# Performance work log

Measured on AMD Instinct MI355X. Metric: run time of the kernel, lower is better.

Reference implementation:

```python
import jax, jax.numpy as jnp
import numpy as np

N = 100000       # nodes
E = 1600000      # edges (avg degree 16)
F_IN = 20        # NUM_FEATURES
H = 128          # hidden_channels
EPS = 1e-5       # GraphNorm eps


def setup_inputs() -> dict:
    key = jax.random.key(0)
    ks = jax.random.split(key, 24)
    s = 0.05
    inp = {
        "x": jax.random.normal(ks[0], (N, F_IN), jnp.float32),
        "edge_index": jax.random.randint(ks[1], (2, E), 0, N, dtype=jnp.int32),
    }
    # SAGEConv params: lin_l (neighbors, with bias), lin_r (root, no bias)
    dims = [(F_IN, H), (H, H), (H, H)]
    k = 2
    for i, (din, dout) in enumerate(dims):
        inp[f"Wl{i}"] = jax.random.normal(ks[k], (dout, din), jnp.float32) * s; k += 1
        inp[f"bl{i}"] = jnp.zeros((dout,), jnp.float32)
        inp[f"Wr{i}"] = jax.random.normal(ks[k], (dout, din), jnp.float32) * s; k += 1
        # GraphNorm: weight, bias, mean_scale (alpha)
        inp[f"gw{i}"] = jnp.ones((dout,), jnp.float32)
        inp[f"gb{i}"] = jnp.zeros((dout,), jnp.float32)
        inp[f"ga{i}"] = jnp.ones((dout,), jnp.float32)
    # MLP head: 128 -> 64 -> 32 -> 1
    inp["hW1"] = jax.random.normal(ks[k], (64, H), jnp.float32) * s; k += 1
    inp["hb1"] = jnp.zeros((64,), jnp.float32)
    inp["hW2"] = jax.random.normal(ks[k], (32, 64), jnp.float32) * s; k += 1
    inp["hb2"] = jnp.zeros((32,), jnp.float32)
    inp["hW3"] = jax.random.normal(ks[k], (1, 32), jnp.float32) * s; k += 1
    inp["hb3"] = jnp.zeros((1,), jnp.float32)
    return inp


def _sage(x, src, dst, Wl, bl, Wr):
    # mean aggregation of source features at destination nodes
    deg = jax.ops.segment_sum(jnp.ones((src.shape[0],), x.dtype), dst, num_segments=N)
    agg = jax.ops.segment_sum(x[src], dst, num_segments=N)
    agg = agg / jnp.maximum(deg, 1.0)[:, None]
    return agg @ Wl.T + bl + x @ Wr.T


def _graphnorm(x, w, b, a):
    # single graph (batch=None): stats over all nodes, per channel
    mean = jnp.mean(x, axis=0)
    c = x - a * mean
    var = jnp.mean(c * c, axis=0)
    return w * c * jax.lax.rsqrt(var + EPS) + b


def reference(x, edge_index,
              Wl0, bl0, Wr0, gw0, gb0, ga0,
              Wl1, bl1, Wr1, gw1, gb1, ga1,
              Wl2, bl2, Wr2, gw2, gb2, ga2,
              hW1, hb1, hW2, hb2, hW3, hb3):
    src, dst = edge_index[0], edge_index[1]
    layers = [(Wl0, bl0, Wr0, gw0, gb0, ga0),
              (Wl1, bl1, Wr1, gw1, gb1, ga1),
              (Wl2, bl2, Wr2, gw2, gb2, ga2)]
    h = x
    for (Wl, bl, Wr, gw, gb, ga) in layers:
        h = _sage(h, src, dst, Wl, bl, Wr)
        h = _graphnorm(h, gw, gb, ga)
        h = jax.nn.gelu(h, approximate=False)  # dropout: eval mode (identity)
    h = jax.nn.gelu(h @ hW1.T + hb1, approximate=False)
    h = jax.nn.gelu(h @ hW2.T + hb2, approximate=False)
    out = jax.nn.sigmoid(h @ hW3.T + hb3)
    return out.squeeze(-1)  # [N]
```

## Files before the change

kernel.cpp:

```cpp
#include <hip/hip_runtime.h>
#include <hip/hip_bf16.h>
#include <math.h>

#define NN 100000
#define EE 1600000
#define FIN 20
#define HH 128
#define NBUK 391
#define FILLB 196
#define MMB 782

typedef __attribute__((ext_vector_type(8))) short bf16x8;
typedef __attribute__((ext_vector_type(4))) float f32x4;

__device__ __forceinline__ unsigned short f2b(float x) {
    unsigned int b = __float_as_uint(x);
    unsigned int r = b + 0x7fffu + ((b >> 16) & 1u);
    return (unsigned short)(r >> 16);
}
__device__ __forceinline__ float lof(unsigned int u) { return __uint_as_float(u << 16); }
__device__ __forceinline__ float hif(unsigned int u) { return __uint_as_float(u & 0xffff0000u); }
__device__ __forceinline__ unsigned int pk2(float a, float b) {
    return (unsigned int)f2b(a) | ((unsigned int)f2b(b) << 16);
}

__device__ __forceinline__ float gelu_exact(float z) {
    return 0.5f * z * (1.0f + erff(z * 0.70710678118654752f));
}

__global__ __launch_bounds__(256) void kb_cnt(const int* __restrict__ dst,
                                              int* __restrict__ bcnt) {
    __shared__ int c[NBUK];
    int t = threadIdx.x;
    for (int i = t; i < NBUK; i += 256) c[i] = 0;
    __syncthreads();
    int e0 = blockIdx.x * 8192;
    #pragma unroll 4
    for (int i = 0; i < 32; ++i) {
        int e = e0 + i * 256 + t;
        if (e < EE) atomicAdd(&c[dst[e] >> 8], 1);
    }
    __syncthreads();
    for (int i = t; i < NBUK; i += 256) if (c[i]) atomicAdd(&bcnt[i], c[i]);
}

__global__ void kb_scan(const int* __restrict__ bcnt, int* __restrict__ bbase,
                        int* __restrict__ cursor) {
    __shared__ int sh[512];
    int t = threadIdx.x;
    int v = (t < NBUK) ? bcnt[t] : 0;
    sh[t] = v;
    __syncthreads();
    for (int off = 1; off < 512; off <<= 1) {
        int add = (t >= off) ? sh[t - off] : 0;
        __syncthreads();
        sh[t] += add;
        __syncthreads();
    }
    if (t < NBUK) {
        int ex = sh[t] - v;
        bbase[t] = ex;
        cursor[t] = ex;
    }
    if (t == NBUK - 1) bbase[NBUK] = sh[t];
}

__global__ __launch_bounds__(256) void kb_fill(const int* __restrict__ src,
        const int* __restrict__ dst, int* __restrict__ cursor,
        unsigned int* __restrict__ pairs) {
    __shared__ int cnt[NBUK], base[NBUK], boff[NBUK];
    int t = threadIdx.x;
    for (int i = t; i < NBUK; i += 256) { cnt[i] = 0; boff[i] = 0; }
    __syncthreads();
    int e0 = blockIdx.x * 8192;
    #pragma unroll 4
    for (int i = 0; i < 32; ++i) {
        int e = e0 + i * 256 + t;
        if (e < EE) atomicAdd(&cnt[dst[e] >> 8], 1);
    }
    __syncthreads();
    for (int i = t; i < NBUK; i += 256)
        if (cnt[i]) base[i] = atomicAdd(&cursor[i], cnt[i]);
    __syncthreads();
    #pragma unroll 4
    for (int i = 0; i < 32; ++i) {
        int e = e0 + i * 256 + t;
        if (e < EE) {
            int d = dst[e];
            int b = d >> 8;
            int pos = base[b] + atomicAdd(&boff[b], 1);
            pairs[pos] = (unsigned int)src[e] | ((unsigned int)(d & 255) << 17);
        }
    }
}

__global__ __launch_bounds__(256) void kb_csr(const unsigned int* __restrict__ pairs,
        const int* __restrict__ bbase, int* __restrict__ row_start,
        int* __restrict__ deg, float* __restrict__ invdeg, int* __restrict__ col) {
    __shared__ int ldeg[256];
    __shared__ int lcnt[256];
    int b = blockIdx.x, t = threadIdx.x;
    int e0 = bbase[b], e1 = bbase[b + 1];
    ldeg[t] = 0;
    lcnt[t] = 0;
    __syncthreads();
    for (int e = e0 + t; e < e1; e += 256) atomicAdd(&ldeg[pairs[e] >> 17], 1);
    __syncthreads();
    int d = ldeg[t];
    for (int off = 1; off < 256; off <<= 1) {
        int add = (t >= off) ? ldeg[t - off] : 0;
        __syncthreads();
        ldeg[t] += add;
        __syncthreads();
    }
    int n = b * 256 + t;
    if (n < NN) {
        row_start[n] = e0 + ldeg[t] - d;
        deg[n] = d;
        invdeg[n] = 1.0f / fmaxf((float)d, 1.0f);
    }
    __syncthreads();
    for (int e = e0 + t; e < e1; e += 256) {
        unsigned int p = pairs[e];
        int dL = p >> 17;
        int pos = e0 + (dL ? ldeg[dL - 1] : 0) + atomicAdd(&lcnt[dL], 1);
        col[pos] = (int)(p & 0x1FFFFu);
    }
}

#define XB_N  (NN * 32)
#define A0_N  (NN * 64)
#define PACK_TOTAL (XB_N + A0_N + 8192 + 32768 + 32768 + 8192 + 2048 + 64 + 32)
__global__ __launch_bounds__(256) void k_pack_all(const float* __restrict__ x,
        const float* __restrict__ Wl0, const float* __restrict__ Wr0,
        const float* __restrict__ Wl1, const float* __restrict__ Wr1,
        const float* __restrict__ Wl2, const float* __restrict__ Wr2,
        const float* __restrict__ hW1, const float* __restrict__ hW2,
        const float* __restrict__ hb1, const float* __restrict__ hb2,
        unsigned short* __restrict__ xb, unsigned short* __restrict__ A0,
        unsigned short* __restrict__ Wt0, unsigned short* __restrict__ Wt2a,
        unsigned short* __restrict__ Wt2b, unsigned short* __restrict__ W1b,
        unsigned short* __restrict__ W2b, float* __restrict__ bH1,
        float* __restrict__ bH2) {
    int id = blockIdx.x * 256 + threadIdx.x;
    if (id < XB_N) {
        int n = id >> 5, k = id & 31;
        xb[id] = f2b((k < FIN) ? x[n * FIN + k] : 0.0f);
        return;
    }
    id -= XB_N;
    if (id < A0_N) {
        int k = id & 63;
        if (k >= FIN) {
            int n = id >> 6;
            float v = (k >= 32 && k < 32 + FIN) ? x[n * FIN + (k - 32)] : 0.0f;
            A0[id] = f2b(v);
        }
        return;
    }
    id -= A0_N;
    if (id < 8192) {
        int c = id >> 6, k = id & 63;
        float v = 0.0f;
        if (k < FIN) v = Wl0[c * FIN + k];
        else if (k >= 32 && k < 32 + FIN) v = Wr0[c * FIN + (k - 32)];
        Wt0[id] = f2b(v);
        return;
    }
    id -= 8192;
    if (id < 32768) {
        int c = id >> 8, k = id & 255;
        Wt2a[id] = f2b((k < HH) ? Wl1[c * HH + k] : Wr1[c * HH + (k - HH)]);
        return;
    }
    id -= 32768;
    if (id < 32768) {
        int c = id >> 8, k = id & 255;
        Wt2b[id] = f2b((k < HH) ? Wl2[c * HH + k] : Wr2[c * HH + (k - HH)]);
        return;
    }
    id -= 32768;
    if (id < 8192) { W1b[id] = f2b(hW1[id]); return; }
    id -= 8192;
    if (id < 2048) { W2b[id] = f2b(hW2[id]); return; }
    id -= 2048;
    if (id < 64) { bH1[id] = hb1[id]; return; }
    id -= 64;
    if (id < 32) { bH2[id] = hb2[id]; return; }
}

__global__ __launch_bounds__(256) void k_agg0(const uint2* __restrict__ xb2,
        const int* __restrict__ rs, const int* __restrict__ deg,
        const float* __restrict__ inv, const int* __restrict__ col,
        unsigned short* __restrict__ A0) {
    int wid = threadIdx.x >> 6;
    int lane = threadIdx.x & 63;
    int er = lane >> 3;
    int c8 = lane & 7;
    int n = blockIdx.x * 4 + wid;
    if (n >= NN) return;
    int s = rs[n], d = deg[n];
    float a0 = 0.f, a1 = 0.f, a2 = 0.f, a3 = 0.f;
    for (int j0 = 0; j0 < d; j0 += 8) {
        int j = j0 + er;
        if (j < d) {
            int c = col[s + j];
            uint2 v = xb2[(size_t)c * 8 + c8];
            a0 += lof(v.x); a1 += hif(v.x);
            a2 += lof(v.y); a3 += hif(v.y);
        }
    }
    #pragma unroll
    for (int m = 8; m < 64; m <<= 1) {
        a0 += __shfl_xor(a0, m, 64);
        a1 += __shfl_xor(a1, m, 64);
        a2 += __shfl_xor(a2, m, 64);
        a3 += __shfl_xor(a3, m, 64);
    }
    if (er == 0 && c8 < 5) {
        float iv = inv[n];
        uint2 o;
        o.x = pk2(a0 * iv, a1 * iv);
        o.y = pk2(a2 * iv, a3 * iv);
        ((uint2*)A0)[(size_t)n * 16 + c8] = o;
    }
}

__global__ __launch_bounds__(256) void k_aggb(const unsigned short* __restrict__ hB,
        const int* __restrict__ rs, const int* __restrict__ deg,
        const float* __restrict__ inv, const int* __restrict__ col,
        unsigned short* __restrict__ aggB) {
    int wid = threadIdx.x >> 6;
    int lane = threadIdx.x & 63;
    int er = lane >> 4;
    int c16 = lane & 15;
    int n = blockIdx.x * 4 + wid;
    if (n >= NN) return;
    int s = rs[n], d = deg[n];
    const uint4* h4 = (const uint4*)hB;
    float a0 = 0.f, a1 = 0.f, a2 = 0.f, a3 = 0.f;
    float a4 = 0.f, a5 = 0.f, a6 = 0.f, a7 = 0.f;
    for (int j0 = 0; j0 < d; j0 += 8) {
        #pragma unroll
        for (int u = 0; u < 2; ++u) {
            int j = j0 + u * 4 + er;
            if (j < d) {
                int c = col[s + j];
                uint4 v = h4[(size_t)c * 16 + c16];
                a0 += lof(v.x); a1 += hif(v.x);
                a2 += lof(v.y); a3 += hif(v.y);
                a4 += lof(v.z); a5 += hif(v.z);
                a6 += lof(v.w); a7 += hif(v.w);
            }
        }
    }
    #pragma unroll
    for (int m = 16; m < 64; m <<= 1) {
        a0 += __shfl_xor(a0, m, 64);
        a1 += __shfl_xor(a1, m, 64);
        a2 += __shfl_xor(a2, m, 64);
        a3 += __shfl_xor(a3, m, 64);
        a4 += __shfl_xor(a4, m, 64);
        a5 += __shfl_xor(a5, m, 64);
        a6 += __shfl_xor(a6, m, 64);
        a7 += __shfl_xor(a7, m, 64);
    }
    if (er == 0) {
        float iv = inv[n];
        uint4 o;
        o.x = pk2(a0 * iv, a1 * iv);
        o.y = pk2(a2 * iv, a3 * iv);
        o.z = pk2(a4 * iv, a5 * iv);
        o.w = pk2(a6 * iv, a7 * iv);
        ((uint4*)aggB)[(size_t)n * 16 + c16] = o;
    }
}

__global__ __launch_bounds__(256) void k_mm(const unsigned short* __restrict__ A0,
        const unsigned short* __restrict__ A1, int c0, int kChunks, int lda,
        const unsigned short* __restrict__ B, int ldb,
        const float* __restrict__ bias, unsigned short* __restrict__ outB,
        float* __restrict__ psPart, float* __restrict__ pqPart, int M) {
    __shared__ __align__(16) unsigned short As[128 * 40];
    __shared__ __align__(16) unsigned short Bs[128 * 40];
    __shared__ float redS[2][128], redQ[2][128];
    const int tid = threadIdx.x;
    const int m0 = blockIdx.x * 128;
    const int w = tid >> 6, lane = tid & 63;
    const int wr = w >> 1, wc = w & 1;
    const int m16 = lane & 15, q = lane >> 4;

    f32x4 acc[4][4];
    #pragma unroll
    for (int i = 0; i < 4; ++i)
        #pragma unroll
        for (int j = 0; j < 4; ++j) acc[i][j] = (f32x4){0.f, 0.f, 0.f, 0.f};

    for (int chunk = 0; chunk < kChunks; ++chunk) {
        const unsigned short* A = (chunk < c0) ? A0 : A1;
        const int kb = (chunk - ((chunk < c0) ? 0 : c0)) * 32;
        #pragma unroll
        for (int it = 0; it < 2; ++it) {
            int s = tid + it * 256;
            int r = s >> 2, p = s & 3;
            int gm = m0 + r;
            uint4 v = make_uint4(0u, 0u, 0u, 0u);
            if (gm < M) v = *(const uint4*)(A + (size_t)gm * lda + kb + p * 8);
            *(uint4*)&As[r * 40 + p * 8] = v;
        }
        {
            const int kbB = chunk * 32;
            #pragma unroll
            for (int it = 0; it < 2; ++it) {
                int s = tid + it * 256;
                int r = s >> 2, p = s & 3;
                uint4 v = *(const uint4*)(B + (size_t)r * ldb + kbB + p * 8);
                *(uint4*)&Bs[r * 40 + p * 8] = v;
            }
        }
        __syncthreads();
        bf16x8 af[4], bfr[4];
        #pragma unroll
        for (int i = 0; i < 4; ++i)
            af[i] = *(const bf16x8*)&As[(wr * 64 + i * 16 + m16) * 40 + q * 8];
        #pragma unroll
        for (int j = 0; j < 4; ++j)
            bfr[j] = *(const bf16x8*)&Bs[(wc * 64 + j * 16 + m16) * 40 + q * 8];
        #pragma unroll
        for (int i = 0; i < 4; ++i)
            #pragma unroll
            for (int j = 0; j < 4; ++j)
                acc[i][j] = __builtin_amdgcn_mfma_f32_16x16x32_bf16(af[i], bfr[j], acc[i][j], 0, 0, 0);
        __syncthreads();
    }

    float cs[4] = {0.f, 0.f, 0.f, 0.f};
    float cq[4] = {0.f, 0.f, 0.f, 0.f};
    #pragma unroll
    for (int i = 0; i < 4; ++i) {
        int mBase = m0 + wr * 64 + i * 16 + q * 4;
        #pragma unroll
        for (int j = 0; j < 4; ++j) {
            int cc = wc * 64 + j * 16 + m16;
            float bv = bias[cc];
            #pragma unroll
            for (int r = 0; r < 4; ++r) {
                int m = mBase + r;
                float v = (m < M) ? (acc[i][j][r] + bv) : 0.0f;
                if (m < M) outB[(size_t)m * 128 + cc] = f2b(v);
                cs[j] += v;
                cq[j] += v * v;
            }
        }
    }
    #pragma unroll
    for (int msk = 16; msk < 64; msk <<= 1) {
        #pragma unroll
        for (int j = 0; j < 4; ++j) {
            cs[j] += __shfl_xor(cs[j], msk, 64);
            cq[j] += __shfl_xor(cq[j], msk, 64);
        }
    }
    if (q == 0) {
        #pragma unroll
        for (int j = 0; j < 4; ++j) {
            int cc = wc * 64 + j * 16 + m16;
            redS[wr][cc] = cs[j];
            redQ[wr][cc] = cq[j];
        }
    }
    __syncthreads();
    if (tid < 128) {
        psPart[(size_t)blockIdx.x * 128 + tid] = redS[0][tid] + redS[1][tid];
        pqPart[(size_t)blockIdx.x * 128 + tid] = redQ[0][tid] + redQ[1][tid];
    }
}

__global__ __launch_bounds__(1024) void k_gn_final(const float* __restrict__ ps,
        const float* __restrict__ pq, const float* __restrict__ gw,
        const float* __restrict__ gb, const float* __restrict__ ga,
        float* __restrict__ cA, float* __restrict__ cB, int nP) {
    __shared__ float shs[8][128], shq[8][128];
    int c = threadIdx.x & 127, sl = threadIdx.x >> 7;
    float s = 0.0f, q = 0.0f;
    for (int b = sl; b < nP; b += 8) {
        s += ps[b * 128 + c];
        q += pq[b * 128 + c];
    }
    shs[sl][c] = s;
    shq[sl][c] = q;
    __syncthreads();
    if (threadIdx.x < 128) {
        float S = 0.0f, Q = 0.0f;
        #pragma unroll
        for (int i = 0; i < 8; ++i) { S += shs[i][c]; Q += shq[i][c]; }
        float mean = S / (float)NN;
        float msq  = Q / (float)NN;
        float a = ga[c];
        float var = msq - mean * mean * a * (2.0f - a);
        float rstd = rsqrtf(var + 1e-5f);
        float A = gw[c] * rstd;
        cA[c] = A;
        cB[c] = gb[c] - a * mean * A;
    }
}

__global__ __launch_bounds__(256) void k_gn_apply(const unsigned short* __restrict__ yB,
        const float* __restrict__ cA, const float* __restrict__ cB,
        unsigned short* __restrict__ hB) {
    int i = blockIdx.x * 256 + threadIdx.x;
    if (i >= NN * 16) return;
    int g = i & 15;
    uint4 v = ((const uint4*)yB)[i];
    float4 A0 = ((const float4*)cA)[g * 2];
    float4 A1 = ((const float4*)cA)[g * 2 + 1];
    float4 B0 = ((const float4*)cB)[g * 2];
    float4 B1 = ((const float4*)cB)[g * 2 + 1];
    unsigned int o0 = pk2(gelu_exact(lof(v.x) * A0.x + B0.x),
                          gelu_exact(hif(v.x) * A0.y + B0.y));
    unsigned int o1 = pk2(gelu_exact(lof(v.y) * A0.z + B0.z),
                          gelu_exact(hif(v.y) * A0.w + B0.w));
    unsigned int o2 = pk2(gelu_exact(lof(v.z) * A1.x + B1.x),
                          gelu_exact(hif(v.z) * A1.y + B1.y));
    unsigned int o3 = pk2(gelu_exact(lof(v.w) * A1.z + B1.z),
                          gelu_exact(hif(v.w) * A1.w + B1.w));
    ((uint4*)hB)[i] = make_uint4(o0, o1, o2, o3);
}

__global__ __launch_bounds__(256) void k_headf(const unsigned short* __restrict__ hB,
        const unsigned short* __restrict__ W1b, const float* __restrict__ b1,
        const unsigned short* __restrict__ W2b, const float* __restrict__ b2,
        const float* __restrict__ W3, const float* __restrict__ b3,
        float* __restrict__ out) {
    __shared__ __align__(16) char pool[23040];
    unsigned short* As  = (unsigned short*)pool;
    unsigned short* Bs  = (unsigned short*)(pool + 10240);
    unsigned short* As2 = (unsigned short*)pool;
    unsigned short* Bs2 = (unsigned short*)(pool + 18432);
    const int tid = threadIdx.x;
    const int m0 = blockIdx.x * 128;
    const int w = tid >> 6, lane = tid & 63;
    const int m16 = lane & 15, q = lane >> 4;

    #pragma unroll
    for (int it = 0; it < 8; ++it) {
        int i = tid + it * 256;
        if (i < 2048) Bs2[(i >> 6) * 72 + (i & 63)] = W2b[i];
    }

    f32x4 acc1[2][4];
    #pragma unroll
    for (int i = 0; i < 2; ++i)
        #pragma unroll
        for (int j = 0; j < 4; ++j) acc1[i][j] = (f32x4){0.f, 0.f, 0.f, 0.f};

    for (int chunk = 0; chunk < 4; ++chunk) {
        const int kb = chunk * 32;
        #pragma unroll
        for (int it = 0; it < 2; ++it) {
            int s = tid + it * 256;
            int r = s >> 2, p = s & 3;
            int gm = m0 + r;
            uint4 v = make_uint4(0u, 0u, 0u, 0u);
            if (gm < NN) v = *(const uint4*)(hB + (size_t)gm * 128 + kb + p * 8);
            *(uint4*)&As[r * 40 + p * 8] = v;
        }
        {
            int r = tid >> 2, p = tid & 3;
            uint4 v = *(const uint4*)(W1b + (size_t)r * 128 + kb + p * 8);
            *(uint4*)&Bs[r * 40 + p * 8] = v;
        }
        __syncthreads();
        bf16x8 af[2], bfr[4];
        #pragma unroll
        for (int i = 0; i < 2; ++i)
            af[i] = *(const bf16x8*)&As[(w * 32 + i * 16 + m16) * 40 + q * 8];
        #pragma unroll
        for (int j = 0; j < 4; ++j)
            bfr[j] = *(const bf16x8*)&Bs[(j * 16 + m16) * 40 + q * 8];
        #pragma unroll
        for (int i = 0; i < 2; ++i)
            #pragma unroll
            for (int j = 0; j < 4; ++j)
                acc1[i][j] = __builtin_amdgcn_mfma_f32_16x16x32_bf16(af[i], bfr[j], acc1[i][j], 0, 0, 0);
        __syncthreads();
    }

    {
        float b1v[4];
        #pragma unroll
        for (int j = 0; j < 4; ++j) b1v[j] = b1[j * 16 + m16];
        #pragma unroll
        for (int i = 0; i < 2; ++i) {
            int mloc = w * 32 + i * 16 + q * 4;
            #pragma unroll
            for (int j = 0; j < 4; ++j) {
                int c = j * 16 + m16;
                #pragma unroll
                for (int r = 0; r < 4; ++r)
                    As2[(mloc + r) * 72 + c] = f2b(gelu_exact(acc1[i][j][r] + b1v[j]));
            }
        }
    }
    __syncthreads();

    f32x4 acc2[2][2];
    #pragma unroll
    for (int i = 0; i < 2; ++i)
        #pragma unroll
        for (int j = 0; j < 2; ++j) acc2[i][j] = (f32x4){0.f, 0.f, 0.f, 0.f};
    #pragma unroll
    for (int kc = 0; kc < 2; ++kc) {
        bf16x8 a2[2], bf2[2];
        #pragma unroll
        for (int i = 0; i < 2; ++i)
            a2[i] = *(const bf16x8*)&As2[(w * 32 + i * 16 + m16) * 72 + kc * 32 + q * 8];
        #pragma unroll
        for (int j = 0; j < 2; ++j)
            bf2[j] = *(const bf16x8*)&Bs2[(j * 16 + m16) * 72 + kc * 32 + q * 8];
        #pragma unroll
        for (int i = 0; i < 2; ++i)
            #pragma unroll
            for (int j = 0; j < 2; ++j)
                acc2[i][j] = __builtin_amdgcn_mfma_f32_16x16x32_bf16(a2[i], bf2[j], acc2[i][j], 0, 0, 0);
    }

    float w3a = W3[m16], w3b = W3[16 + m16];
    float b2a = b2[m16], b2b = b2[16 + m16];
    float p[8];
    #pragma unroll
    for (int i = 0; i < 2; ++i)
        #pragma unroll
        for (int r = 0; r < 4; ++r) {
            float za = gelu_exact(acc2[i][0][r] + b2a);
            float zb = gelu_exact(acc2[i][1][r] + b2b);
            p[i * 4 + r] = za * w3a + zb * w3b;
        }
    #pragma unroll
    for (int msk = 1; msk < 16; msk <<= 1)
        #pragma unroll
        for (int k = 0; k < 8; ++k) p[k] += __shfl_xor(p[k], msk, 64);
    if (m16 == 0) {
        float b3v = b3[0];
        #pragma unroll
        for (int i = 0; i < 2; ++i)
            #pragma unroll
            for (int r = 0; r < 4; ++r) {
                int m = m0 + w * 32 + i * 16 + q * 4 + r;
                if (m < NN) out[m] = 1.0f / (1.0f + expf(-(p[i * 4 + r] + b3v)));
            }
    }
}

extern "C" void kernel_launch(void* const* d_in, const int* in_sizes, int n_in,
                              void* d_out, int out_size, void* d_ws, size_t ws_size,
                              hipStream_t stream) {
    const float* x   = (const float*)d_in[0];
    const int*   ei  = (const int*)d_in[1];
    const float* Wl0 = (const float*)d_in[2];
    const float* bl0 = (const float*)d_in[3];
    const float* Wr0 = (const float*)d_in[4];
    const float* gw0 = (const float*)d_in[5];
    const float* gb0 = (const float*)d_in[6];
    const float* ga0 = (const float*)d_in[7];
    const float* Wl1 = (const float*)d_in[8];
    const float* bl1 = (const float*)d_in[9];
    const float* Wr1 = (const float*)d_in[10];
    const float* gw1 = (const float*)d_in[11];
    const float* gb1 = (const float*)d_in[12];
    const float* ga1 = (const float*)d_in[13];
    const float* Wl2 = (const float*)d_in[14];
    const float* bl2 = (const float*)d_in[15];
    const float* Wr2 = (const float*)d_in[16];
    const float* gw2 = (const float*)d_in[17];
    const float* gb2 = (const float*)d_in[18];
    const float* ga2 = (const float*)d_in[19];
    const float* hW1 = (const float*)d_in[20];
    const float* hb1 = (const float*)d_in[21];
    const float* hW2 = (const float*)d_in[22];
    const float* hb2 = (const float*)d_in[23];
    const float* hW3 = (const float*)d_in[24];
    const float* hb3 = (const float*)d_in[25];
    float* out = (float*)d_out;

    size_t off = 0;
    auto carve = [&](size_t bytes) -> void* {
        void* p = (void*)((char*)d_ws + off);
        off += (bytes + 255) & ~(size_t)255;
        return p;
    };
    int*   bcnt      = (int*)carve((size_t)NBUK * 4);
    int*   bbase     = (int*)carve((size_t)(NBUK + 1) * 4);
    int*   cursor    = (int*)carve((size_t)NBUK * 4);
    unsigned int* pairs = (unsigned int*)carve((size_t)EE * 4);
    int*   deg       = (int*)carve((size_t)NN * 4);
    int*   row_start = (int*)carve((size_t)NN * 4);
    float* invdeg    = (float*)carve((size_t)NN * 4);
    int*   colarr    = (int*)carve((size_t)EE * 4);
    unsigned short* xb    = (unsigned short*)carve((size_t)NN * 32 * 2);
    unsigned short* Wt0   = (unsigned short*)carve(128 * 64 * 2);
    unsigned short* Wt2a  = (unsigned short*)carve(128 * 256 * 2);
    unsigned short* Wt2b  = (unsigned short*)carve(128 * 256 * 2);
    unsigned short* W1b   = (unsigned short*)carve(64 * 128 * 2);
    unsigned short* W2b   = (unsigned short*)carve(32 * 64 * 2);
    float* biasH1    = (float*)carve(64 * 4);
    float* biasH2    = (float*)carve(32 * 4);
    float* ps        = (float*)carve((size_t)MMB * 128 * 4);
    float* pq        = (float*)carve((size_t)MMB * 128 * 4);
    float* coefA     = (float*)carve(128 * 4);
    float* coefB     = (float*)carve(128 * 4);
    unsigned short* A0pack = (unsigned short*)carve((size_t)NN * 64 * 2);
    unsigned short* hB   = (unsigned short*)carve((size_t)NN * HH * 2);
    unsigned short* aggB = (unsigned short*)carve((size_t)NN * HH * 2);
    unsigned short* yB   = (unsigned short*)carve((size_t)NN * HH * 2);
    if (off > ws_size) return;

    const int* src = ei;
    const int* dst = ei + EE;

    hipMemsetAsync(bcnt, 0, (size_t)NBUK * 4, stream);
    k_pack_all<<<(PACK_TOTAL + 255) / 256, 256, 0, stream>>>(
        x, Wl0, Wr0, Wl1, Wr1, Wl2, Wr2, hW1, hW2, hb1, hb2,
        xb, A0pack, Wt0, Wt2a, Wt2b, W1b, W2b, biasH1, biasH2);
    kb_cnt<<<FILLB, 256, 0, stream>>>(dst, bcnt);
    kb_scan<<<1, 512, 0, stream>>>(bcnt, bbase, cursor);
    kb_fill<<<FILLB, 256, 0, stream>>>(src, dst, cursor, pairs);
    kb_csr<<<NBUK, 256, 0, stream>>>(pairs, bbase, row_start, deg, invdeg, colarr);

    k_agg0<<<(NN + 3) / 4, 256, 0, stream>>>((const uint2*)xb, row_start,
                                             deg, invdeg, colarr, A0pack);
    k_mm<<<MMB, 256, 0, stream>>>(A0pack, A0pack, 2, 2, 64, Wt0, 64, bl0, yB, ps, pq, NN);
    k_gn_final<<<1, 1024, 0, stream>>>(ps, pq, gw0, gb0, ga0, coefA, coefB, MMB);
    k_gn_apply<<<(NN * 16 + 255) / 256, 256, 0, stream>>>(yB, coefA, coefB, hB);

    const unsigned short* WtL[2] = {Wt2a, Wt2b};
    const float* blL[2] = {bl1, bl2};
    const float* gwL[2] = {gw1, gw2};
    const float* gbL[2] = {gb1, gb2};
    const float* gaL[2] = {ga1, ga2};
    for (int l = 0; l < 2; ++l) {
        k_aggb<<<(NN + 3) / 4, 256, 0, stream>>>(hB, row_start, deg, invdeg, colarr, aggB);
        k_mm<<<MMB, 256, 0, stream>>>(aggB, hB, 4, 8, 128, WtL[l], 256, blL[l],
                                      yB, ps, pq, NN);
        k_gn_final<<<1, 1024, 0, stream>>>(ps, pq, gwL[l], gbL[l], gaL[l], coefA, coefB, MMB);
        k_gn_apply<<<(NN * 16 + 255) / 256, 256, 0, stream>>>(yB, coefA, coefB, hB);
    }

    k_headf<<<MMB, 256, 0, stream>>>(hB, W1b, biasH1, W2b, biasH2, hW3, hb3, out);
}
```

Baseline: 587.7 us.

## Store hidden features channel-chunked to shrink gather working set in aggregation

Hidden activations and aggregated features now use a channel-chunked layout: 8 slabs of 16 bf16 channels, each NN rows by 32 bytes. The aggregation kernel runs 8 times as many blocks, each covering one channel chunk, so the randomly gathered working set per pass is a 3.2MB slab that can stay in cache instead of the full 25.6MB feature matrix. The matmul, GraphNorm apply and head kernels are changed to read and write this layout, and the second-layer matmul becomes a specialized k_mmc kernel. The tradeoffs are 32-byte gather granularity in place of 256-byte rows, more blocks that each re-read the CSR and degree arrays, and strided A-tile loads in the matmul.

Result: slower. 899.8 us (+53.1%).

```diff
diff --git a/kernel.cpp b/kernel.cpp
--- a/kernel.cpp
+++ b/kernel.cpp
@@ -226,59 +226,42 @@
     }
 }
 
-__global__ __launch_bounds__(256) void k_aggb(const unsigned short* __restrict__ hB,
+__global__ __launch_bounds__(256) void k_aggb(const unsigned int* __restrict__ hC,
         const int* __restrict__ rs, const int* __restrict__ deg,
         const float* __restrict__ inv, const int* __restrict__ col,
-        unsigned short* __restrict__ aggB) {
+        unsigned int* __restrict__ aggC) {
+    int cc  = blockIdx.x & 7;
+    int grp = blockIdx.x >> 3;
     int wid = threadIdx.x >> 6;
     int lane = threadIdx.x & 63;
-    int er = lane >> 4;
-    int c16 = lane & 15;
-    int n = blockIdx.x * 4 + wid;
+    int er = lane >> 3;
+    int c8 = lane & 7;
+    int n = grp * 4 + wid;
     if (n >= NN) return;
     int s = rs[n], d = deg[n];
-    const uint4* h4 = (const uint4*)hB;
-    float a0 = 0.f, a1 = 0.f, a2 = 0.f, a3 = 0.f;
-    float a4 = 0.f, a5 = 0.f, a6 = 0.f, a7 = 0.f;
-    for (int j0 = 0; j0 < d; j0 += 8) {
-        #pragma unroll
-        for (int u = 0; u < 2; ++u) {
-            int j = j0 + u * 4 + er;
-            if (j < d) {
-                int c = col[s + j];
-                uint4 v = h4[(size_t)c * 16 + c16];
-                a0 += lof(v.x); a1 += hif(v.x);
-                a2 += lof(v.y); a3 += hif(v.y);
-                a4 += lof(v.z); a5 += hif(v.z);
-                a6 += lof(v.w); a7 += hif(v.w);
-            }
-        }
-    }
-    #pragma unroll
-    for (int m = 16; m < 64; m <<= 1) {
+    const unsigned int* base = hC + (size_t)cc * NN * 8 + c8;
+    float a0 = 0.f, a1 = 0.f;
+    for (int j0 = 0; j0 < d; j0 += 16) {
+        int j1 = j0 + er, j2 = j0 + 8 + er;
+        unsigned int u1 = 0u, u2 = 0u;
+        if (j1 < d) u1 = base[(size_t)col[s + j1] * 8];
+        if (j2 < d) u2 = base[(size_t)col[s + j2] * 8];
+        a0 += lof(u1) + lof(u2);
+        a1 += hif(u1) + hif(u2);
+    }
+    #pragma unroll
+    for (int m = 8; m < 64; m <<= 1) {
         a0 += __shfl_xor(a0, m, 64);
         a1 += __shfl_xor(a1, m, 64);
-        a2 += __shfl_xor(a2, m, 64);
-        a3 += __shfl_xor(a3, m, 64);
-        a4 += __shfl_xor(a4, m, 64);
-        a5 += __shfl_xor(a5, m, 64);
-        a6 += __shfl_xor(a6, m, 64);
-        a7 += __shfl_xor(a7, m, 64);
     }
     if (er == 0) {
         float iv = inv[n];
-        uint4 o;
-        o.x = pk2(a0 * iv, a1 * iv);
-        o.y = pk2(a2 * iv, a3 * iv);
-        o.z = pk2(a4 * iv, a5 * iv);
-        o.w = pk2(a6 * iv, a7 * iv);
-        ((uint4*)aggB)[(size_t)n * 16 + c16] = o;
+        aggC[((size_t)cc * NN + n) * 8 + c8] = pk2(a0 * iv, a1 * iv);
     }
 }
 
 __global__ __launch_bounds__(256) void k_mm(const unsigned short* __restrict__ A0,
-        const unsigned short* __restrict__ A1, int c0, int kChunks, int lda,
-        const unsigned short* __restrict__ B, int ldb,
+        int kChunks, int lda, const unsigned short* __restrict__ B, int ldb,
         const float* __restrict__ bias, unsigned short* __restrict__ outB,
         float* __restrict__ psPart, float* __restrict__ pqPart, int M) {
     __shared__ __align__(16) unsigned short As[128 * 40];
@@ -297,15 +280,110 @@
         for (int j = 0; j < 4; ++j) acc[i][j] = (f32x4){0.f, 0.f, 0.f, 0.f};
 
     for (int chunk = 0; chunk < kChunks; ++chunk) {
-        const unsigned short* A = (chunk < c0) ? A0 : A1;
-        const int kb = (chunk - ((chunk < c0) ? 0 : c0)) * 32;
+        const int kb = chunk * 32;
         #pragma unroll
         for (int it = 0; it < 2; ++it) {
             int s = tid + it * 256;
             int r = s >> 2, p = s & 3;
             int gm = m0 + r;
             uint4 v = make_uint4(0u, 0u, 0u, 0u);
-            if (gm < M) v = *(const uint4*)(A + (size_t)gm * lda + kb + p * 8);
+            if (gm < M) v = *(const uint4*)(A0 + (size_t)gm * lda + kb + p * 8);
+            *(uint4*)&As[r * 40 + p * 8] = v;
+        }
+        #pragma unroll
+        for (int it = 0; it < 2; ++it) {
+            int s = tid + it * 256;
+            int r = s >> 2, p = s & 3;
+            uint4 v = *(const uint4*)(B + (size_t)r * ldb + kb + p * 8);
+            *(uint4*)&Bs[r * 40 + p * 8] = v;
+        }
+        __syncthreads();
+        bf16x8 af[4], bfr[4];
+        #pragma unroll
+        for (int i = 0; i < 4; ++i)
+            af[i] = *(const bf16x8*)&As[(wr * 64 + i * 16 + m16) * 40 + q * 8];
+        #pragma unroll
+        for (int j = 0; j < 4; ++j)
+            bfr[j] = *(const bf16x8*)&Bs[(wc * 64 + j * 16 + m16) * 40 + q * 8];
+        #pragma unroll
+        for (int i = 0; i < 4; ++i)
+            #pragma unroll
+            for (int j = 0; j < 4; ++j)
+                acc[i][j] = __builtin_amdgcn_mfma_f32_16x16x32_bf16(af[i], bfr[j], acc[i][j], 0, 0, 0);
+        __syncthreads();
+    }
+
+    float cs[4] = {0.f, 0.f, 0.f, 0.f};
+    float cq[4] = {0.f, 0.f, 0.f, 0.f};
+    #pragma unroll
+    for (int i = 0; i < 4; ++i) {
+        int mBase = m0 + wr * 64 + i * 16 + q * 4;
+        #pragma unroll
+        for (int j = 0; j < 4; ++j) {
+            int cc = wc * 64 + j * 16 + m16;
+            float bv = bias[cc];
+            #pragma unroll
+            for (int r = 0; r < 4; ++r) {
+                int m = mBase + r;
+                float v = (m < M) ? (acc[i][j][r] + bv) : 0.0f;
+                if (m < M) outB[(size_t)m * 128 + cc] = f2b(v);
+                cs[j] += v;
+                cq[j] += v * v;
+            }
+        }
+    }
+    #pragma unroll
+    for (int msk = 16; msk < 64; msk <<= 1) {
+        #pragma unroll
+        for (int j = 0; j < 4; ++j) {
+            cs[j] += __shfl_xor(cs[j], msk, 64);
+            cq[j] += __shfl_xor(cq[j], msk, 64);
+        }
+    }
+    if (q == 0) {
+        #pragma unroll
+        for (int j = 0; j < 4; ++j) {
+            int cc = wc * 64 + j * 16 + m16;
+            redS[wr][cc] = cs[j];
+            redQ[wr][cc] = cq[j];
+        }
+    }
+    __syncthreads();
+    if (tid < 128) {
+        psPart[(size_t)blockIdx.x * 128 + tid] = redS[0][tid] + redS[1][tid];
+        pqPart[(size_t)blockIdx.x * 128 + tid] = redQ[0][tid] + redQ[1][tid];
+    }
+}
+
+__global__ __launch_bounds__(256) void k_mmc(const uint4* __restrict__ aggC4,
+        const uint4* __restrict__ hC4, const unsigned short* __restrict__ B,
+        const float* __restrict__ bias, unsigned short* __restrict__ outB,
+        float* __restrict__ psPart, float* __restrict__ pqPart, int M) {
+    __shared__ __align__(16) unsigned short As[128 * 40];
+    __shared__ __align__(16) unsigned short Bs[128 * 40];
+    __shared__ float redS[2][128], redQ[2][128];
+    const int tid = threadIdx.x;
+    const int m0 = blockIdx.x * 128;
+    const int w = tid >> 6, lane = tid & 63;
+    const int wr = w >> 1, wc = w & 1;
+    const int m16 = lane & 15, q = lane >> 4;
+
+    f32x4 acc[4][4];
+    #pragma unroll
+    for (int i = 0; i < 4; ++i)
+        #pragma unroll
+        for (int j = 0; j < 4; ++j) acc[i][j] = (f32x4){0.f, 0.f, 0.f, 0.f};
+
+    for (int chunk = 0; chunk < 8; ++chunk) {
+        const uint4* Asrc = (chunk < 4) ? aggC4 : hC4;
+        const int cb = (chunk & 3) * 2;
+        #pragma unroll
+        for (int it = 0; it < 2; ++it) {
+            int s = tid + it * 256;
+            int r = s >> 2, p = s & 3;
+            int gm = m0 + r;
+            uint4 v = make_uint4(0u, 0u, 0u, 0u);
+            if (gm < M) v = Asrc[((size_t)(cb + (p >> 1)) * NN + gm) * 2 + (p & 1)];
             *(uint4*)&As[r * 40 + p * 8] = v;
         }
         {
@@ -314,7 +392,7 @@
             for (int it = 0; it < 2; ++it) {
                 int s = tid + it * 256;
                 int r = s >> 2, p = s & 3;
-                uint4 v = *(const uint4*)(B + (size_t)r * ldb + kbB + p * 8);
+                uint4 v = *(const uint4*)(B + (size_t)r * 256 + kbB + p * 8);
                 *(uint4*)&Bs[r * 40 + p * 8] = v;
             }
         }
@@ -407,9 +485,10 @@
 
 __global__ __launch_bounds__(256) void k_gn_apply(const unsigned short* __restrict__ yB,
         const float* __restrict__ cA, const float* __restrict__ cB,
-        unsigned short* __restrict__ hB) {
+        uint4* __restrict__ hC4) {
     int i = blockIdx.x * 256 + threadIdx.x;
     if (i >= NN * 16) return;
+    int n = i >> 4;
     int g = i & 15;
     uint4 v = ((const uint4*)yB)[i];
     float4 A0 = ((const float4*)cA)[g * 2];
@@ -424,10 +503,10 @@
                           gelu_exact(hif(v.z) * A1.y + B1.y));
     unsigned int o3 = pk2(gelu_exact(lof(v.w) * A1.z + B1.z),
                           gelu_exact(hif(v.w) * A1.w + B1.w));
-    ((uint4*)hB)[i] = make_uint4(o0, o1, o2, o3);
-}
-
-__global__ __launch_bounds__(256) void k_headf(const unsigned short* __restrict__ hB,
+    hC4[((size_t)(g >> 1) * NN + n) * 2 + (g & 1)] = make_uint4(o0, o1, o2, o3);
+}
+
+__global__ __launch_bounds__(256) void k_headf(const uint4* __restrict__ hC4,
         const unsigned short* __restrict__ W1b, const float* __restrict__ b1,
         const unsigned short* __restrict__ W2b, const float* __restrict__ b2,
         const float* __restrict__ W3, const float* __restrict__ b3,
@@ -462,7 +541,7 @@
             int r = s >> 2, p = s & 3;
             int gm = m0 + r;
             uint4 v = make_uint4(0u, 0u, 0u, 0u);
-            if (gm < NN) v = *(const uint4*)(hB + (size_t)gm * 128 + kb + p * 8);
+            if (gm < NN) v = hC4[((size_t)(chunk * 2 + (p >> 1)) * NN + gm) * 2 + (p & 1)];
             *(uint4*)&As[r * 40 + p * 8] = v;
         }
         {
@@ -610,9 +689,9 @@
     float* coefA     = (float*)carve(128 * 4);
     float* coefB     = (float*)carve(128 * 4);
     unsigned short* A0pack = (unsigned short*)carve((size_t)NN * 64 * 2);
-    unsigned short* hB   = (unsigned short*)carve((size_t)NN * HH * 2);
-    unsigned short* aggB = (unsigned short*)carve((size_t)NN * HH * 2);
-    unsigned short* yB   = (unsigned short*)carve((size_t)NN * HH * 2);
+    unsigned int* hC   = (unsigned int*)carve((size_t)NN * HH * 2);
+    unsigned int* aggC = (unsigned int*)carve((size_t)NN * HH * 2);
+    unsigned short* yB = (unsigned short*)carve((size_t)NN * HH * 2);
     if (off > ws_size) return;
 
     const int* src = ei;
@@ -629,9 +708,9 @@
 
     k_agg0<<<(NN + 3) / 4, 256, 0, stream>>>((const uint2*)xb, row_start,
                                              deg, invdeg, colarr, A0pack);
-    k_mm<<<MMB, 256, 0, stream>>>(A0pack, A0pack, 2, 2, 64, Wt0, 64, bl0, yB, ps, pq, NN);
+    k_mm<<<MMB, 256, 0, stream>>>(A0pack, 2, 64, Wt0, 64, bl0, yB, ps, pq, NN);
     k_gn_final<<<1, 1024, 0, stream>>>(ps, pq, gw0, gb0, ga0, coefA, coefB, MMB);
-    k_gn_apply<<<(NN * 16 + 255) / 256, 256, 0, stream>>>(yB, coefA, coefB, hB);
+    k_gn_apply<<<(NN * 16 + 255) / 256, 256, 0, stream>>>(yB, coefA, coefB, (uint4*)hC);
 
     const unsigned short* WtL[2] = {Wt2a, Wt2b};
     const float* blL[2] = {bl1, bl2};
@@ -639,12 +718,14 @@
     const float* gbL[2] = {gb1, gb2};
     const float* gaL[2] = {ga1, ga2};
     for (int l = 0; l < 2; ++l) {
-        k_aggb<<<(NN + 3) / 4, 256, 0, stream>>>(hB, row_start, deg, invdeg, colarr, aggB);
-        k_mm<<<MMB, 256, 0, stream>>>(aggB, hB, 4, 8, 128, WtL[l], 256, blL[l],
-                                      yB, ps, pq, NN);
+        k_aggb<<<((NN + 3) / 4) * 8, 256, 0, stream>>>(hC, row_start, deg, invdeg,
+                                                       colarr, aggC);
+        k_mmc<<<MMB, 256, 0, stream>>>((const uint4*)aggC, (const uint4*)hC,
+                                       WtL[l], blL[l], yB, ps, pq, NN);
         k_gn_final<<<1, 1024, 0, stream>>>(ps, pq, gwL[l], gbL[l], gaL[l], coefA, coefB, MMB);
-        k_gn_apply<<<(NN * 16 + 255) / 256, 256, 0, stream>>>(yB, coefA, coefB, hB);
-    }
-
-    k_headf<<<MMB, 256, 0, stream>>>(hB, W1b, biasH1, W2b, biasH2, hW3, hb3, out);
-}
+        k_gn_apply<<<(NN * 16 + 255) / 256, 256, 0, stream>>>(yB, coefA, coefB, (uint4*)hC);
+    }
+
+    k_headf<<<MMB, 256, 0, stream>>>((const uint4*)hC, W1b, biasH1, W2b, biasH2,
+                                     hW3, hb3, out);
+}
```

## Fuse GraphNorm reduction into matmul, fold last norm into head, rework aggregation

Applied to the files above, without the earlier changes.

The matmul kernel now accumulates GraphNorm column sums with global atomics, and the last block to finish (detected through a ticket counter) computes the normalization coefficients. This removes the separate single-block reduction kernels. The final layer's norm-and-GELU apply pass is folded into the head kernel's A-tile load, and the bcnt memset is moved into the pack kernel along with zeroing the new accumulators. Neighbor aggregation switches to one 64-thread block per node, each thread handling two channels with a 4-way unrolled gather. In exchange, float atomic accumulation makes the statistics order-nondeterministic, and launching one block per node adds per-block scheduling overhead.

Measured after the change: 734.5 us. 25.0% more time.

```diff
diff --git a/kernel.cpp b/kernel.cpp
--- a/kernel.cpp
+++ b/kernel.cpp
@@ -130,7 +130,7 @@
 
 #define XB_N  (NN * 32)
 #define A0_N  (NN * 64)
-#define PACK_TOTAL (XB_N + A0_N + 8192 + 32768 + 32768 + 8192 + 2048 + 64 + 32)
+#define PACK_TOTAL (XB_N + A0_N + 8192 + 32768 + 32768 + 8192 + 2048 + 64 + 32 + NBUK + 8 + 768)
 __global__ __launch_bounds__(256) void k_pack_all(const float* __restrict__ x,
         const float* __restrict__ Wl0, const float* __restrict__ Wr0,
         const float* __restrict__ Wl1, const float* __restrict__ Wr1,
@@ -141,7 +141,8 @@
         unsigned short* __restrict__ Wt0, unsigned short* __restrict__ Wt2a,
         unsigned short* __restrict__ Wt2b, unsigned short* __restrict__ W1b,
         unsigned short* __restrict__ W2b, float* __restrict__ bH1,
-        float* __restrict__ bH2) {
+        float* __restrict__ bH2, int* __restrict__ bcnt, int* __restrict__ ticks,
+        float* __restrict__ gnS) {
     int id = blockIdx.x * 256 + threadIdx.x;
     if (id < XB_N) {
         int n = id >> 5, k = id & 31;
@@ -187,6 +188,12 @@
     if (id < 64) { bH1[id] = hb1[id]; return; }
     id -= 64;
     if (id < 32) { bH2[id] = hb2[id]; return; }
+    id -= 32;
+    if (id < NBUK) { bcnt[id] = 0; return; }
+    id -= NBUK;
+    if (id < 8) { ticks[id] = 0; return; }
+    id -= 8;
+    if (id < 768) { gnS[id] = 0.0f; return; }
 }
 
 __global__ __launch_bounds__(256) void k_agg0(const uint2* __restrict__ xb2,
@@ -226,64 +233,47 @@
     }
 }
 
-__global__ __launch_bounds__(256) void k_aggb(const unsigned short* __restrict__ hB,
+__global__ __launch_bounds__(64) void k_aggb(const unsigned short* __restrict__ hB,
         const int* __restrict__ rs, const int* __restrict__ deg,
         const float* __restrict__ inv, const int* __restrict__ col,
         unsigned short* __restrict__ aggB) {
-    int wid = threadIdx.x >> 6;
-    int lane = threadIdx.x & 63;
-    int er = lane >> 4;
-    int c16 = lane & 15;
-    int n = blockIdx.x * 4 + wid;
-    if (n >= NN) return;
+    int n = blockIdx.x;
+    int t = threadIdx.x;
     int s = rs[n], d = deg[n];
-    const uint4* h4 = (const uint4*)hB;
-    float a0 = 0.f, a1 = 0.f, a2 = 0.f, a3 = 0.f;
-    float a4 = 0.f, a5 = 0.f, a6 = 0.f, a7 = 0.f;
-    for (int j0 = 0; j0 < d; j0 += 8) {
-        #pragma unroll
-        for (int u = 0; u < 2; ++u) {
-            int j = j0 + u * 4 + er;
-            if (j < d) {
-                int c = col[s + j];
-                uint4 v = h4[(size_t)c * 16 + c16];
-                a0 += lof(v.x); a1 += hif(v.x);
-                a2 += lof(v.y); a3 += hif(v.y);
-                a4 += lof(v.z); a5 += hif(v.z);
-                a6 += lof(v.w); a7 += hif(v.w);
-            }
-        }
-    }
-    #pragma unroll
-    for (int m = 16; m < 64; m <<= 1) {
-        a0 += __shfl_xor(a0, m, 64);
-        a1 += __shfl_xor(a1, m, 64);
-        a2 += __shfl_xor(a2, m, 64);
-        a3 += __shfl_xor(a3, m, 64);
-        a4 += __shfl_xor(a4, m, 64);
-        a5 += __shfl_xor(a5, m, 64);
-        a6 += __shfl_xor(a6, m, 64);
-        a7 += __shfl_xor(a7, m, 64);
-    }
-    if (er == 0) {
-        float iv = inv[n];
-        uint4 o;
-        o.x = pk2(a0 * iv, a1 * iv);
-        o.y = pk2(a2 * iv, a3 * iv);
-        o.z = pk2(a4 * iv, a5 * iv);
-        o.w = pk2(a6 * iv, a7 * iv);
-        ((uint4*)aggB)[(size_t)n * 16 + c16] = o;
-    }
+    const unsigned int* h32 = (const unsigned int*)hB;
+    float a0 = 0.0f, a1 = 0.0f;
+    int j = 0;
+    for (; j + 3 < d; j += 4) {
+        int c0 = col[s + j], c1 = col[s + j + 1];
+        int c2 = col[s + j + 2], c3 = col[s + j + 3];
+        unsigned int u0 = h32[(size_t)c0 * 64 + t];
+        unsigned int u1 = h32[(size_t)c1 * 64 + t];
+        unsigned int u2 = h32[(size_t)c2 * 64 + t];
+        unsigned int u3 = h32[(size_t)c3 * 64 + t];
+        a0 += lof(u0) + lof(u1) + lof(u2) + lof(u3);
+        a1 += hif(u0) + hif(u1) + hif(u2) + hif(u3);
+    }
+    for (; j < d; ++j) {
+        unsigned int u = h32[(size_t)col[s + j] * 64 + t];
+        a0 += lof(u);
+        a1 += hif(u);
+    }
+    float iv = inv[n];
+    ((unsigned int*)aggB)[(size_t)n * 64 + t] = pk2(a0 * iv, a1 * iv);
 }
 
 __global__ __launch_bounds__(256) void k_mm(const unsigned short* __restrict__ A0,
         const unsigned short* __restrict__ A1, int c0, int kChunks, int lda,
         const unsigned short* __restrict__ B, int ldb,
         const float* __restrict__ bias, unsigned short* __restrict__ outB,
-        float* __restrict__ psPart, float* __restrict__ pqPart, int M) {
+        float* __restrict__ ps, float* __restrict__ pq, int* __restrict__ tick,
+        const float* __restrict__ gw, const float* __restrict__ gb,
+        const float* __restrict__ ga, float* __restrict__ cA,
+        float* __restrict__ cB, int M) {
     __shared__ __align__(16) unsigned short As[128 * 40];
     __shared__ __align__(16) unsigned short Bs[128 * 40];
     __shared__ float redS[2][128], redQ[2][128];
+    __shared__ int lastFlag;
     const int tid = threadIdx.x;
     const int m0 = blockIdx.x * 128;
     const int w = tid >> 6, lane = tid & 63;
@@ -371,37 +361,24 @@
     }
     __syncthreads();
     if (tid < 128) {
-        psPart[(size_t)blockIdx.x * 128 + tid] = redS[0][tid] + redS[1][tid];
-        pqPart[(size_t)blockIdx.x * 128 + tid] = redQ[0][tid] + redQ[1][tid];
-    }
-}
-
-__global__ __launch_bounds__(1024) void k_gn_final(const float* __restrict__ ps,
-        const float* __restrict__ pq, const float* __restrict__ gw,
-        const float* __restrict__ gb, const float* __restrict__ ga,
-        float* __restrict__ cA, float* __restrict__ cB, int nP) {
-    __shared__ float shs[8][128], shq[8][128];
-    int c = threadIdx.x & 127, sl = threadIdx.x >> 7;
-    float s = 0.0f, q = 0.0f;
-    for (int b = sl; b < nP; b += 8) {
-        s += ps[b * 128 + c];
-        q += pq[b * 128 + c];
-    }
-    shs[sl][c] = s;
-    shq[sl][c] = q;
-    __syncthreads();
-    if (threadIdx.x < 128) {
-        float S = 0.0f, Q = 0.0f;
-        #pragma unroll
-        for (int i = 0; i < 8; ++i) { S += shs[i][c]; Q += shq[i][c]; }
+        atomicAdd(&ps[tid], redS[0][tid] + redS[1][tid]);
+        atomicAdd(&pq[tid], redQ[0][tid] + redQ[1][tid]);
+    }
+    __threadfence();
+    __syncthreads();
+    if (tid == 0) lastFlag = (atomicAdd(tick, 1) == (int)gridDim.x - 1);
+    __syncthreads();
+    if (lastFlag && tid < 128) {
+        float S = atomicAdd(&ps[tid], 0.0f);
+        float Q = atomicAdd(&pq[tid], 0.0f);
         float mean = S / (float)NN;
         float msq  = Q / (float)NN;
-        float a = ga[c];
+        float a = ga[tid];
         float var = msq - mean * mean * a * (2.0f - a);
         float rstd = rsqrtf(var + 1e-5f);
-        float A = gw[c] * rstd;
-        cA[c] = A;
-        cB[c] = gb[c] - a * mean * A;
+        float A = gw[tid] * rstd;
+        cA[tid] = A;
+        cB[tid] = gb[tid] - a * mean * A;
     }
 }
 
@@ -427,7 +404,8 @@
     ((uint4*)hB)[i] = make_uint4(o0, o1, o2, o3);
 }
 
-__global__ __launch_bounds__(256) void k_headf(const unsigned short* __restrict__ hB,
+__global__ __launch_bounds__(256) void k_headf(const unsigned short* __restrict__ yB,
+        const float* __restrict__ cAp, const float* __restrict__ cBp,
         const unsigned short* __restrict__ W1b, const float* __restrict__ b1,
         const unsigned short* __restrict__ W2b, const float* __restrict__ b2,
         const float* __restrict__ W3, const float* __restrict__ b3,
@@ -441,6 +419,8 @@
     const int m0 = blockIdx.x * 128;
     const int w = tid >> 6, lane = tid & 63;
     const int m16 = lane & 15, q = lane >> 4;
+    const float4* cA4 = (const float4*)cAp;
+    const float4* cB4 = (const float4*)cBp;
 
     #pragma unroll
     for (int it = 0; it < 8; ++it) {
@@ -462,8 +442,20 @@
             int r = s >> 2, p = s & 3;
             int gm = m0 + r;
             uint4 v = make_uint4(0u, 0u, 0u, 0u);
-            if (gm < NN) v = *(const uint4*)(hB + (size_t)gm * 128 + kb + p * 8);
-            *(uint4*)&As[r * 40 + p * 8] = v;
+            if (gm < NN) v = *(const uint4*)(yB + (size_t)gm * 128 + kb + p * 8);
+            int cg = chunk * 8 + p * 2;
+            float4 Ax = cA4[cg], Ay = cA4[cg + 1];
+            float4 Bx = cB4[cg], By = cB4[cg + 1];
+            uint4 o;
+            o.x = pk2(gelu_exact(lof(v.x) * Ax.x + Bx.x),
+                      gelu_exact(hif(v.x) * Ax.y + Bx.y));
+            o.y = pk2(gelu_exact(lof(v.y) * Ax.z + Bx.z),
+                      gelu_exact(hif(v.y) * Ax.w + Bx.w));
+            o.z = pk2(gelu_exact(lof(v.z) * Ay.x + By.x),
+                      gelu_exact(hif(v.z) * Ay.y + By.y));
+            o.w = pk2(gelu_exact(lof(v.w) * Ay.z + By.z),
+                      gelu_exact(hif(v.w) * Ay.w + By.w));
+            *(uint4*)&As[r * 40 + p * 8] = o;
         }
         {
             int r = tid >> 2, p = tid & 3;
@@ -605,10 +597,10 @@
     unsigned short* W2b   = (unsigned short*)carve(32 * 64 * 2);
     float* biasH1    = (float*)carve(64 * 4);
     float* biasH2    = (float*)carve(32 * 4);
-    float* ps        = (float*)carve((size_t)MMB * 128 * 4);
-    float* pq        = (float*)carve((size_t)MMB * 128 * 4);
-    float* coefA     = (float*)carve(128 * 4);
-    float* coefB     = (float*)carve(128 * 4);
+    float* gnS       = (float*)carve(768 * 4);
+    int*   ticks     = (int*)carve(8 * 4);
+    float* cAall     = (float*)carve(3 * 128 * 4);
+    float* cBall     = (float*)carve(3 * 128 * 4);
     unsigned short* A0pack = (unsigned short*)carve((size_t)NN * 64 * 2);
     unsigned short* hB   = (unsigned short*)carve((size_t)NN * HH * 2);
     unsigned short* aggB = (unsigned short*)carve((size_t)NN * HH * 2);
@@ -618,10 +610,10 @@
     const int* src = ei;
     const int* dst = ei + EE;
 
-    hipMemsetAsync(bcnt, 0, (size_t)NBUK * 4, stream);
     k_pack_all<<<(PACK_TOTAL + 255) / 256, 256, 0, stream>>>(
         x, Wl0, Wr0, Wl1, Wr1, Wl2, Wr2, hW1, hW2, hb1, hb2,
-        xb, A0pack, Wt0, Wt2a, Wt2b, W1b, W2b, biasH1, biasH2);
+        xb, A0pack, Wt0, Wt2a, Wt2b, W1b, W2b, biasH1, biasH2,
+        bcnt, ticks, gnS);
     kb_cnt<<<FILLB, 256, 0, stream>>>(dst, bcnt);
     kb_scan<<<1, 512, 0, stream>>>(bcnt, bbase, cursor);
     kb_fill<<<FILLB, 256, 0, stream>>>(src, dst, cursor, pairs);
@@ -629,22 +621,22 @@
 
     k_agg0<<<(NN + 3) / 4, 256, 0, stream>>>((const uint2*)xb, row_start,
                                              deg, invdeg, colarr, A0pack);
-    k_mm<<<MMB, 256, 0, stream>>>(A0pack, A0pack, 2, 2, 64, Wt0, 64, bl0, yB, ps, pq, NN);
-    k_gn_final<<<1, 1024, 0, stream>>>(ps, pq, gw0, gb0, ga0, coefA, coefB, MMB);
-    k_gn_apply<<<(NN * 16 + 255) / 256, 256, 0, stream>>>(yB, coefA, coefB, hB);
-
-    const unsigned short* WtL[2] = {Wt2a, Wt2b};
-    const float* blL[2] = {bl1, bl2};
-    const float* gwL[2] = {gw1, gw2};
-    const float* gbL[2] = {gb1, gb2};
-    const float* gaL[2] = {ga1, ga2};
-    for (int l = 0; l < 2; ++l) {
-        k_aggb<<<(NN + 3) / 4, 256, 0, stream>>>(hB, row_start, deg, invdeg, colarr, aggB);
-        k_mm<<<MMB, 256, 0, stream>>>(aggB, hB, 4, 8, 128, WtL[l], 256, blL[l],
-                                      yB, ps, pq, NN);
-        k_gn_final<<<1, 1024, 0, stream>>>(ps, pq, gwL[l], gbL[l], gaL[l], coefA, coefB, MMB);
-        k_gn_apply<<<(NN * 16 + 255) / 256, 256, 0, stream>>>(yB, coefA, coefB, hB);
-    }
-
-    k_headf<<<MMB, 256, 0, stream>>>(hB, W1b, biasH1, W2b, biasH2, hW3, hb3, out);
-}
+    k_mm<<<MMB, 256, 0, stream>>>(A0pack, A0pack, 2, 2, 64, Wt0, 64, bl0, yB,
+                                  gnS + 0, gnS + 128, ticks + 0,
+                                  gw0, gb0, ga0, cAall + 0, cBall + 0, NN);
+    k_gn_apply<<<(NN * 16 + 255) / 256, 256, 0, stream>>>(yB, cAall + 0, cBall + 0, hB);
+
+    k_aggb<<<NN, 64, 0, stream>>>(hB, row_start, deg, invdeg, colarr, aggB);
+    k_mm<<<MMB, 256, 0, stream>>>(aggB, hB, 4, 8, 128, Wt2a, 256, bl1, yB,
+                                  gnS + 256, gnS + 384, ticks + 1,
+                                  gw1, gb1, ga1, cAall + 128, cBall + 128, NN);
+    k_gn_apply<<<(NN * 16 + 255) / 256, 256, 0, stream>>>(yB, cAall + 128, cBall + 128, hB);
+
+    k_aggb<<<NN, 64, 0, stream>>>(hB, row_start, deg, invdeg, colarr, aggB);
+    k_mm<<<MMB, 256, 0, stream>>>(aggB, hB, 4, 8, 128, Wt2b, 256, bl2, yB,
+                                  gnS + 512, gnS + 640, ticks + 2,
+                                  gw2, gb2, ga2, cAall + 256, cBall + 256, NN);
+
+    k_headf<<<MMB, 256, 0, stream>>>(yB, cAall + 256, cBall + 256,
+                                     W1b, biasH1, W2b, biasH2, hW3, hb3, out);
+}
```
